# Kernel optimization log

Measured on AMD Instinct MI355X. Metric: run time of the kernel, lower is better.

## Reference

```python
import jax, jax.numpy as jnp
import numpy as np

TOPK = 3  # matches init_kwargs topk


def setup_inputs() -> dict:
    key = jax.random.key(0)
    k1, k2, k3 = jax.random.split(key, 3)
    B, N, D, E, L = 256, 1024, 1024, 8, 1000
    features = jax.random.normal(k1, (B, N, D), dtype=jnp.float32)
    gate_w = jax.random.normal(k2, (D, E), dtype=jnp.float32) * (1.0 / np.sqrt(D))
    gate_b = jnp.zeros((E,), dtype=jnp.float32)
    cls_w = jax.random.normal(k3, (E, L, D), dtype=jnp.float32) * (1.0 / np.sqrt(D))
    cls_b = jnp.zeros((E, L), dtype=jnp.float32)
    return {"features": features, "gate_w": gate_w, "gate_b": gate_b,
            "cls_w": cls_w, "cls_b": cls_b}


def reference(features, gate_w, gate_b, cls_w, cls_b):
    # features: [B, N, D]; gate_w: [D, E]; cls_w: [E, L, D]
    B = features.shape[0]
    E = cls_w.shape[0]
    gate_score = features @ gate_w + gate_b                      # [B, N, E]
    gate_prob = jax.nn.softmax(gate_score.transpose(0, 2, 1), axis=-1)  # [B, E, N] softmax over tokens
    top_v, top_i = jax.lax.top_k(gate_prob, TOPK)                # [B, E, K]
    # gather top-k token features per expert -> [B, E, K, D]
    gathered = features[jnp.arange(B)[:, None, None], top_i]
    comb_w = jax.nn.softmax(top_v, axis=-1)                      # [B, E, K]
    # per-expert linear: [B, E, K, L]
    logits = jnp.einsum('bekd,eld->bekl', gathered, cls_w) + cls_b[None, :, None, :]
    # weighted sum over K, then mean over experts -> [B, L]
    out = jnp.einsum('bekl,bek->bl', logits, comb_w) / E
    return out
```

## Files before the change

### kernel.cpp

```cpp
#include <hip/hip_runtime.h>
#include <hip/hip_bf16.h>
#include <cfloat>

#define B_ 256
#define N_ 1024
#define D_ 1024
#define E_ 8
#define L_ 1000

typedef float f32x4 __attribute__((ext_vector_type(4)));
typedef short bf16x8 __attribute__((ext_vector_type(8)));

__device__ inline unsigned short f2bf(float f) {
  unsigned u = __builtin_bit_cast(unsigned, f);
  u += 0x7fffu + ((u >> 16) & 1u);
  return (unsigned short)(u >> 16);
}

__global__ __launch_bounds__(256, 8) void k_gate(const float* __restrict__ feat,
                                                 const float* __restrict__ gate_w,
                                                 float* __restrict__ scores) {
  __shared__ float gwT[E_ * D_];
  __shared__ float sm[8][17];
  const int t = threadIdx.x;
#pragma unroll
  for (int j = 0; j < 32; ++j) {
    int idx = j * 256 + t;
    gwT[(idx & 7) * D_ + (idx >> 3)] = gate_w[idx];
  }
  __syncthreads();

  const int wave = t >> 6, lane = t & 63;
  const long rowBase = ((long)blockIdx.x * 4 + wave) * 4;
  const float* fbase = feat + rowBase * D_ + lane * 4;

  float acc[32];
#pragma unroll
  for (int j = 0; j < 32; ++j) acc[j] = 0.f;

#pragma unroll 1
  for (int it = 0; it < 4; ++it) {
    const int d0 = it * 256;
    float4 f[4];
#pragma unroll
    for (int r = 0; r < 4; ++r) f[r] = *(const float4*)(fbase + r * D_ + d0);
#pragma unroll
    for (int e = 0; e < 8; ++e) {
      const float4 g = *(const float4*)(&gwT[e * D_ + d0 + lane * 4]);
#pragma unroll
      for (int r = 0; r < 4; ++r) {
        acc[r * 8 + e] = fmaf(f[r].x, g.x,
                         fmaf(f[r].y, g.y,
                         fmaf(f[r].z, g.z,
                         fmaf(f[r].w, g.w, acc[r * 8 + e]))));
      }
    }
  }

#pragma unroll
  for (int s = 0; s < 5; ++s) {
    const int m = 1 << s;
    const int half = 16 >> s;
    const bool up = (lane & m) != 0;
#pragma unroll
    for (int j = 0; j < half; ++j) {
      float keep = up ? acc[j + half] : acc[j];
      float send = up ? acc[j] : acc[j + half];
      acc[j] = keep + __shfl_xor(send, m, 64);
    }
  }
  acc[0] += __shfl_xor(acc[0], 32, 64);
  const int L5 = lane & 31;
  const int v = ((L5 & 1) << 4) | ((L5 & 2) << 2) | (L5 & 4) |
                ((L5 & 8) >> 2) | ((L5 & 16) >> 4);
  if (lane < 32) sm[v & 7][wave * 4 + (v >> 3)] = acc[0];
  __syncthreads();
  if (t < 128) {
    const int te = t >> 4, tr = t & 15;
    scores[(size_t)te * (B_ * N_) + (size_t)blockIdx.x * 16 + tr] = sm[te][tr];
  }
}

__global__ __launch_bounds__(256) void k_topk_gather(
    const float* __restrict__ scores, const float* __restrict__ feat,
    unsigned short* __restrict__ wf) {
  __shared__ int sI[3];
  __shared__ float sC[3];
  const int t = threadIdx.x, w = t >> 6, lane = t & 63;
  const int pair = blockIdx.x;
  const int b = pair >> 3, e = pair & 7;

  if (w == 0) {
    const float* s = scores + (size_t)e * (B_ * N_) + (size_t)b * N_;
    float v[16];
#pragma unroll
    for (int j = 0; j < 4; ++j) {
      const float4 x = *(const float4*)(s + j * 256 + lane * 4);
      v[j * 4 + 0] = x.x; v[j * 4 + 1] = x.y;
      v[j * 4 + 2] = x.z; v[j * 4 + 3] = x.w;
    }

    float M[3];
    int I[3];
    float Z = 0.f;
#pragma unroll
    for (int k = 0; k < 3; ++k) {
      float lm = -FLT_MAX;
      int ln = 0x7fffffff;
#pragma unroll
      for (int j = 0; j < 4; ++j)
#pragma unroll
        for (int c = 0; c < 4; ++c) {
          const float val = v[j * 4 + c];
          if (val > lm) { lm = val; ln = j * 256 + lane * 4 + c; }
        }
#pragma unroll
      for (int s2 = 1; s2 < 64; s2 <<= 1) {
        float om = __shfl_xor(lm, s2, 64);
        int on = __shfl_xor(ln, s2, 64);
        if (om > lm || (om == lm && on < ln)) { lm = om; ln = on; }
      }
      M[k] = lm;
      I[k] = ln;
      if (k == 0) {
        float se = 0.f;
#pragma unroll
        for (int j = 0; j < 16; ++j) se += expf(v[j] - lm);
#pragma unroll
        for (int s2 = 1; s2 < 64; s2 <<= 1) se += __shfl_xor(se, s2, 64);
        Z = se;
      }
      const int slot = ln >> 8, owner = (ln >> 2) & 63, comp = ln & 3;
#pragma unroll
      for (int j = 0; j < 4; ++j)
#pragma unroll
        for (int c = 0; c < 4; ++c)
          if (j == slot && c == comp && owner == lane)
            v[j * 4 + c] = -FLT_MAX;
    }

    if (lane == 0) {
      const float p0 = 1.f / Z;
      const float p1 = expf(M[1] - M[0]) / Z;
      const float p2 = expf(M[2] - M[0]) / Z;
      const float c1 = expf(p1 - p0);
      const float c2 = expf(p2 - p0);
      const float den = 1.f + c1 + c2;
      sI[0] = I[0]; sI[1] = I[1]; sI[2] = I[2];
      sC[0] = 1.f / den; sC[1] = c1 / den; sC[2] = c2 / den;
    }
  }
  __syncthreads();

  const int i0 = sI[0], i1 = sI[1], i2 = sI[2];
  const float c0 = sC[0], c1 = sC[1], c2 = sC[2];
  const float* f = feat + (size_t)b * N_ * D_;
  const int d = t * 4;
  const float4 x = *(const float4*)(f + (size_t)i0 * D_ + d);
  const float4 y = *(const float4*)(f + (size_t)i1 * D_ + d);
  const float4 z = *(const float4*)(f + (size_t)i2 * D_ + d);
  ushort4 o;
  o.x = f2bf(c0 * x.x + c1 * y.x + c2 * z.x);
  o.y = f2bf(c0 * x.y + c1 * y.y + c2 * z.y);
  o.z = f2bf(c0 * x.z + c1 * y.z + c2 * z.z);
  o.w = f2bf(c0 * x.w + c1 * y.w + c2 * z.w);
  *(ushort4*)(wf + (size_t)pair * D_ + d) = o;
}

__global__ __launch_bounds__(512) void k_cls(const unsigned short* __restrict__ wf,
                                             const float* __restrict__ cls_w,
                                             float* __restrict__ part) {
  __shared__ uint4 Ag[2][128 * 8];
  __shared__ uint4 Bg[2][64 * 8];

  const int bx = blockIdx.x;
  const int e = bx >> 5, bt = (bx >> 4) & 1, lt = bx & 15;
  const int m0 = bt * 128, l0 = lt * 64;
  const int t = threadIdx.x;
  const int w = t >> 6, lane = t & 63;
  const int wm = w >> 1, wn = w & 1;

  const int ar = t >> 2, ag2 = t & 3;
  const int br = t >> 3, bq = t & 7;
  const int lg = (l0 + br < L_) ? (l0 + br) : (L_ - 1);
  const unsigned short* agp = wf + ((size_t)(m0 + ar) * E_ + e) * D_ + ag2 * 16;
  const float* bgp = cls_w + ((size_t)e * L_ + lg) * D_ + bq * 8;

  uint4 areg[2];
  float4 breg[2];

  auto load_regs = [&](int step) {
    const int d0 = step * 64;
    areg[0] = *(const uint4*)(agp + d0);
    areg[1] = *(const uint4*)(agp + d0 + 8);
    breg[0] = *(const float4*)(bgp + d0);
    breg[1] = *(const float4*)(bgp + d0 + 4);
  };

  auto write_lds = [&](int c) {
#pragma unroll
    for (int j = 0; j < 2; ++j)
      Ag[c][ar * 8 + ((ag2 * 2 + j) ^ (ar & 7))] = areg[j];
    uint4 p;
    p.x = (unsigned)f2bf(breg[0].x) | ((unsigned)f2bf(breg[0].y) << 16);
    p.y = (unsigned)f2bf(breg[0].z) | ((unsigned)f2bf(breg[0].w) << 16);
    p.z = (unsigned)f2bf(breg[1].x) | ((unsigned)f2bf(breg[1].y) << 16);
    p.w = (unsigned)f2bf(breg[1].z) | ((unsigned)f2bf(breg[1].w) << 16);
    Bg[c][br * 8 + (bq ^ (br & 7))] = p;
  };

  f32x4 acc[2][2];
#pragma unroll
  for (int m = 0; m < 2; ++m)
#pragma unroll
    for (int n = 0; n < 2; ++n) acc[m][n] = (f32x4){0.f, 0.f, 0.f, 0.f};

  const int l15 = lane & 15, lhi = lane >> 4;

  load_regs(0);
  for (int step = 0; step < 16; ++step) {
    const int c = step & 1;
    write_lds(c);
    if (step < 15) load_regs(step + 1);
    __syncthreads();
#pragma unroll
    for (int ks = 0; ks < 2; ++ks) {
      bf16x8 a[2], b[2];
#pragma unroll
      for (int m = 0; m < 2; ++m) {
        const int row = wm * 32 + m * 16 + l15;
        a[m] = __builtin_bit_cast(bf16x8,
                 Ag[c][row * 8 + ((ks * 4 + lhi) ^ (row & 7))]);
      }
#pragma unroll
      for (int n = 0; n < 2; ++n) {
        const int row = wn * 32 + n * 16 + l15;
        b[n] = __builtin_bit_cast(bf16x8,
                 Bg[c][row * 8 + ((ks * 4 + lhi) ^ (row & 7))]);
      }
#pragma unroll
      for (int m = 0; m < 2; ++m)
#pragma unroll
        for (int n = 0; n < 2; ++n)
          acc[m][n] = __builtin_amdgcn_mfma_f32_16x16x32_bf16(
              a[m], b[n], acc[m][n], 0, 0, 0);
    }
    __syncthreads();
  }

#pragma unroll
  for (int m = 0; m < 2; ++m) {
#pragma unroll
    for (int n = 0; n < 2; ++n) {
      const int col = l0 + wn * 32 + n * 16 + l15;
      if (col < L_) {
#pragma unroll
        for (int j = 0; j < 4; ++j) {
          const int row = m0 + wm * 32 + m * 16 + lhi * 4 + j;
          part[((size_t)e * B_ + row) * L_ + col] = acc[m][n][j];
        }
      }
    }
  }
}

__global__ __launch_bounds__(256) void k_reduce(const float* __restrict__ part,
                                                const float* __restrict__ cls_b,
                                                float* __restrict__ out) {
  const int idx = blockIdx.x * 256 + threadIdx.x;
  if (idx >= B_ * L_) return;
  const int l = idx % L_;
  float s = 0.f, bias = 0.f;
#pragma unroll
  for (int e = 0; e < 8; ++e) {
    s += part[(long)e * (B_ * L_) + idx];
    bias += cls_b[e * L_ + l];
  }
  out[idx] = (s + bias) * 0.125f;
}

extern "C" void kernel_launch(void* const* d_in, const int* in_sizes, int n_in,
                              void* d_out, int out_size, void* d_ws, size_t ws_size,
                              hipStream_t stream) {
  const float* feat   = (const float*)d_in[0];
  const float* gate_w = (const float*)d_in[1];
  const float* cls_w  = (const float*)d_in[3];
  const float* cls_b  = (const float*)d_in[4];
  float* out = (float*)d_out;

  char* ws = (char*)d_ws;
  float*          scores = (float*)ws;
  float*          part   = (float*)ws;
  unsigned short* wfb    = (unsigned short*)(ws + 8388608);

  k_gate<<<16384, 256, 0, stream>>>(feat, gate_w, scores);
  k_topk_gather<<<2048, 256, 0, stream>>>(scores, feat, wfb);
  k_cls<<<256, 512, 0, stream>>>(wfb, cls_w, part);
  k_reduce<<<1000, 256, 0, stream>>>(part, cls_b, out);
}
```

Baseline: 246.9 us.

## Double-buffer feature loads in gate kernel and process 32 rows per block

The gate kernel now has each wave handle 8 rows in two groups of 4 and walks 8 chunks with register double-buffering: the next chunk's float4 feature loads are issued before the current chunk's FMAs. Launching half as many blocks spreads the shared-memory transpose of gate_w over twice the rows, and that staging now uses float4 global loads. The aim is to hide global-memory latency in this bandwidth-bound pass over the 1 GB feature tensor. In exchange it uses more registers (occupancy hint dropped) and a larger shared-memory staging array.

Measured after the change: 664.6 us. +169.2%, slower.

```diff
diff --git a/kernel.cpp b/kernel.cpp
--- a/kernel.cpp
+++ b/kernel.cpp
@@ -17,68 +17,86 @@
   return (unsigned short)(u >> 16);
 }
 
-__global__ __launch_bounds__(256, 8) void k_gate(const float* __restrict__ feat,
-                                                 const float* __restrict__ gate_w,
-                                                 float* __restrict__ scores) {
+__global__ __launch_bounds__(256) void k_gate(const float* __restrict__ feat,
+                                              const float* __restrict__ gate_w,
+                                              float* __restrict__ scores) {
   __shared__ float gwT[E_ * D_];
-  __shared__ float sm[8][17];
+  __shared__ float sm[8][132];
   const int t = threadIdx.x;
-#pragma unroll
-  for (int j = 0; j < 32; ++j) {
-    int idx = j * 256 + t;
-    gwT[(idx & 7) * D_ + (idx >> 3)] = gate_w[idx];
+  const float4* gw4 = (const float4*)gate_w;
+#pragma unroll
+  for (int j = 0; j < 8; ++j) {
+    const int idx4 = j * 256 + t;
+    const float4 v = gw4[idx4];
+    const int d = idx4 >> 1, e0 = (idx4 & 1) * 4;
+    gwT[(e0 + 0) * D_ + d] = v.x;
+    gwT[(e0 + 1) * D_ + d] = v.y;
+    gwT[(e0 + 2) * D_ + d] = v.z;
+    gwT[(e0 + 3) * D_ + d] = v.w;
   }
   __syncthreads();
 
   const int wave = t >> 6, lane = t & 63;
-  const long rowBase = ((long)blockIdx.x * 4 + wave) * 4;
+  const long rowBase = ((long)blockIdx.x * 4 + wave) * 8;
   const float* fbase = feat + rowBase * D_ + lane * 4;
 
-  float acc[32];
-#pragma unroll
-  for (int j = 0; j < 32; ++j) acc[j] = 0.f;
-
-#pragma unroll 1
-  for (int it = 0; it < 4; ++it) {
-    const int d0 = it * 256;
-    float4 f[4];
-#pragma unroll
-    for (int r = 0; r < 4; ++r) f[r] = *(const float4*)(fbase + r * D_ + d0);
-#pragma unroll
-    for (int e = 0; e < 8; ++e) {
-      const float4 g = *(const float4*)(&gwT[e * D_ + d0 + lane * 4]);
-#pragma unroll
-      for (int r = 0; r < 4; ++r) {
-        acc[r * 8 + e] = fmaf(f[r].x, g.x,
-                         fmaf(f[r].y, g.y,
-                         fmaf(f[r].z, g.z,
-                         fmaf(f[r].w, g.w, acc[r * 8 + e]))));
-      }
-    }
-  }
-
-#pragma unroll
-  for (int s = 0; s < 5; ++s) {
-    const int m = 1 << s;
-    const int half = 16 >> s;
-    const bool up = (lane & m) != 0;
-#pragma unroll
-    for (int j = 0; j < half; ++j) {
-      float keep = up ? acc[j + half] : acc[j];
-      float send = up ? acc[j] : acc[j + half];
-      acc[j] = keep + __shfl_xor(send, m, 64);
-    }
-  }
-  acc[0] += __shfl_xor(acc[0], 32, 64);
   const int L5 = lane & 31;
   const int v = ((L5 & 1) << 4) | ((L5 & 2) << 2) | (L5 & 4) |
                 ((L5 & 8) >> 2) | ((L5 & 16) >> 4);
-  if (lane < 32) sm[v & 7][wave * 4 + (v >> 3)] = acc[0];
+
+  float4 f[2][4];
+#pragma unroll
+  for (int r = 0; r < 4; ++r) f[0][r] = *(const float4*)(fbase + r * D_);
+
+  float acc[32];
+#pragma unroll
+  for (int j = 0; j < 32; ++j) acc[j] = 0.f;
+
+#pragma unroll
+  for (int c = 0; c < 8; ++c) {
+    const int cur = c & 1;
+    if (c < 7) {
+      const int cn = c + 1, gn = cn >> 2, itn = cn & 3;
+#pragma unroll
+      for (int r = 0; r < 4; ++r)
+        f[cur ^ 1][r] = *(const float4*)(fbase + (gn * 4 + r) * D_ + itn * 256);
+    }
+    const int g = c >> 2, it = c & 3;
+#pragma unroll
+    for (int e = 0; e < 8; ++e) {
+      const float4 gv = *(const float4*)(&gwT[e * D_ + it * 256 + lane * 4]);
+#pragma unroll
+      for (int r = 0; r < 4; ++r) {
+        acc[r * 8 + e] = fmaf(f[cur][r].x, gv.x,
+                         fmaf(f[cur][r].y, gv.y,
+                         fmaf(f[cur][r].z, gv.z,
+                         fmaf(f[cur][r].w, gv.w, acc[r * 8 + e]))));
+      }
+    }
+    if (it == 3) {
+#pragma unroll
+      for (int s = 0; s < 5; ++s) {
+        const int m = 1 << s;
+        const int half = 16 >> s;
+        const bool up = (lane & m) != 0;
+#pragma unroll
+        for (int j = 0; j < half; ++j) {
+          float keep = up ? acc[j + half] : acc[j];
+          float send = up ? acc[j] : acc[j + half];
+          acc[j] = keep + __shfl_xor(send, m, 64);
+        }
+      }
+      acc[0] += __shfl_xor(acc[0], 32, 64);
+      if (lane < 32) sm[v & 7][wave * 8 + g * 4 + (v >> 3)] = acc[0];
+      if (c < 7) {
+#pragma unroll
+        for (int j = 0; j < 32; ++j) acc[j] = 0.f;
+      }
+    }
+  }
   __syncthreads();
-  if (t < 128) {
-    const int te = t >> 4, tr = t & 15;
-    scores[(size_t)te * (B_ * N_) + (size_t)blockIdx.x * 16 + tr] = sm[te][tr];
-  }
+  const int te = t >> 5, tr = t & 31;
+  scores[(size_t)te * (B_ * N_) + (long)blockIdx.x * 32 + tr] = sm[te][tr];
 }
 
 __global__ __launch_bounds__(256) void k_topk_gather(
@@ -293,7 +311,7 @@
   float*          part   = (float*)ws;
   unsigned short* wfb    = (unsigned short*)(ws + 8388608);
 
-  k_gate<<<16384, 256, 0, stream>>>(feat, gate_w, scores);
+  k_gate<<<8192, 256, 0, stream>>>(feat, gate_w, scores);
   k_topk_gather<<<2048, 256, 0, stream>>>(scores, feat, wfb);
   k_cls<<<256, 512, 0, stream>>>(wfb, cls_w, part);
   k_reduce<<<1000, 256, 0, stream>>>(part, cls_b, out);
```
